# Optimization experiments

Measured on AMD Instinct MI355X. Metric: run time of the kernel, lower is better.

Reference implementation:

```python
import jax, jax.numpy as jnp
import numpy as np
import math

DEPTH = 6
D_MODEL = 512
N_HEADS = 8
D_HEAD = D_MODEL // N_HEADS
D_FF = 2048
SEQ_LEN = 2048
VOCAB = 256
B, T = 2, 2048
EPS = 1e-5


def setup_inputs() -> dict:
    key = jax.random.key(0)
    ks = jax.random.split(key, 16)
    std = 0.02
    std_proj = 0.02 / math.sqrt(2 * DEPTH)
    inp = {
        "x": jax.random.randint(ks[0], (B, T), 0, VOCAB, dtype=jnp.int64)
             if jax.config.jax_enable_x64 else
             jax.random.randint(ks[0], (B, T), 0, VOCAB, dtype=jnp.int32),
        "tok_emb": std * jax.random.normal(ks[1], (VOCAB, D_MODEL), jnp.float32),
        "pos_emb": std * jax.random.normal(ks[2], (SEQ_LEN, D_MODEL), jnp.float32),
        "qkv_w": std * jax.random.normal(ks[3], (DEPTH, 3 * D_MODEL, D_MODEL), jnp.float32),
        "proj_w": std_proj * jax.random.normal(ks[4], (DEPTH, D_MODEL, D_MODEL), jnp.float32),
        "ln1_w": jnp.ones((DEPTH, D_MODEL), jnp.float32),
        "ln1_b": jnp.zeros((DEPTH, D_MODEL), jnp.float32),
        "ln2_w": jnp.ones((DEPTH, D_MODEL), jnp.float32),
        "ln2_b": jnp.zeros((DEPTH, D_MODEL), jnp.float32),
        "fc1_w": std * jax.random.normal(ks[5], (DEPTH, D_FF, D_MODEL), jnp.float32),
        "fc2_w": std_proj * jax.random.normal(ks[6], (DEPTH, D_MODEL, D_FF), jnp.float32),
        "lnf_w": jnp.ones((D_MODEL,), jnp.float32),
        "lnf_b": jnp.zeros((D_MODEL,), jnp.float32),
        "head_w": std * jax.random.normal(ks[7], (VOCAB, D_MODEL), jnp.float32),
    }
    return inp


def _layernorm(x, w, b):
    mu = jnp.mean(x, axis=-1, keepdims=True)
    var = jnp.mean(jnp.square(x - mu), axis=-1, keepdims=True)
    return (x - mu) * jax.lax.rsqrt(var + EPS) * w + b


def _attention(x, qkv_w, proj_w):
    Bq, Tq, d = x.shape
    qkv = jnp.einsum('btd,ed->bte', x, qkv_w)  # [B,T,3d]
    q, k, v = jnp.split(qkv, 3, axis=-1)
    def split(t):
        return t.reshape(Bq, Tq, N_HEADS, D_HEAD).transpose(0, 2, 1, 3)  # [B,H,T,Dh]
    q, k, v = split(q), split(k), split(v)
    scores = jnp.einsum('bhqd,bhkd->bhqk', q, k) / math.sqrt(D_HEAD)
    mask = jnp.tril(jnp.ones((Tq, Tq), dtype=bool))
    scores = jnp.where(mask, scores, -jnp.inf)
    attn = jax.nn.softmax(scores, axis=-1)
    out = jnp.einsum('bhqk,bhkd->bhqd', attn, v)
    out = out.transpose(0, 2, 1, 3).reshape(Bq, Tq, d)
    return jnp.einsum('btd,ed->bte', out, proj_w)


def reference(x, tok_emb, pos_emb, qkv_w, proj_w, ln1_w, ln1_b, ln2_w, ln2_b,
              fc1_w, fc2_w, lnf_w, lnf_b, head_w):
    Tq = x.shape[1]
    h = tok_emb[x] + pos_emb[:Tq][None, :, :]  # [B,T,d]
    for l in range(DEPTH):
        a = _attention(_layernorm(h, ln1_w[l], ln1_b[l]), qkv_w[l], proj_w[l])
        h = h + a
        m = _layernorm(h, ln2_w[l], ln2_b[l])
        m = jax.nn.gelu(jnp.einsum('btd,fd->btf', m, fc1_w[l]), approximate=False)
        h = h + jnp.einsum('btf,df->btd', m, fc2_w[l])
    h = _layernorm(h, lnf_w, lnf_b)
    return jnp.einsum('btd,vd->btv', h, head_w)  # [B,T,VOCAB]
```

## Files before the change

### kernel.cpp

```cpp
#include <hip/hip_runtime.h>
#include <hip/hip_bf16.h>
#include <math.h>

typedef __hip_bfloat16 bf16;
typedef __attribute__((ext_vector_type(8))) short short8;
typedef __attribute__((ext_vector_type(4))) float f32x4;

#define DEPTH 6
#define DM    512
#define NH    8
#define DH    64
#define DFF   2048
#define TSEQ  2048
#define BATCH 2
#define ROWS  (BATCH*TSEQ)
#define NVOCAB 256

#define Q3_K_OFF  2097152
#define Q3_VT_OFF 4194304

constexpr size_t SZ_QKV  = (size_t)DEPTH * 3 * DM * DM;
constexpr size_t SZ_PROJ = (size_t)DEPTH * DM * DM;
constexpr size_t SZ_FC1  = (size_t)DEPTH * DFF * DM;
constexpr size_t SZ_FC2  = SZ_FC1;
constexpr size_t SZ_HEAD = (size_t)NVOCAB * DM;
constexpr size_t SZ_ALL  = SZ_QKV + SZ_PROJ + SZ_FC1 + SZ_FC2 + SZ_HEAD;

#define GLDS(gp, lp) __builtin_amdgcn_global_load_lds( \
    (const __attribute__((address_space(1))) void*)(gp), \
    (__attribute__((address_space(3))) void*)(lp), 16, 0, 0)

__device__ __forceinline__ short f2bs(float x) {
    union { bf16 b; short s; } u; u.b = __float2bfloat16(x); return u.s;
}

__global__ __launch_bounds__(256) void w2b_all(const float* __restrict__ q,
    const float* __restrict__ p, const float* __restrict__ f1,
    const float* __restrict__ f2, const float* __restrict__ hw, bf16* __restrict__ dst)
{
    size_t i = ((size_t)blockIdx.x * 256 + threadIdx.x) * 8;
    const float* s; size_t off;
    if      (i < SZ_QKV)                               { s = q;  off = 0; }
    else if (i < SZ_QKV + SZ_PROJ)                     { s = p;  off = SZ_QKV; }
    else if (i < SZ_QKV + SZ_PROJ + SZ_FC1)            { s = f1; off = SZ_QKV + SZ_PROJ; }
    else if (i < SZ_QKV + SZ_PROJ + SZ_FC1 + SZ_FC2)   { s = f2; off = SZ_QKV + SZ_PROJ + SZ_FC1; }
    else                                               { s = hw; off = SZ_QKV + SZ_PROJ + SZ_FC1 + SZ_FC2; }
    float4 f0 = *(const float4*)(s + (i - off));
    float4 f1v = *(const float4*)(s + (i - off) + 4);
    short8 o;
    o[0] = f2bs(f0.x); o[1] = f2bs(f0.y); o[2] = f2bs(f0.z); o[3] = f2bs(f0.w);
    o[4] = f2bs(f1v.x); o[5] = f2bs(f1v.y); o[6] = f2bs(f1v.z); o[7] = f2bs(f1v.w);
    *(short8*)((short*)dst + i) = o;
}

__global__ __launch_bounds__(256) void emb_kernel(const int* __restrict__ x,
    const float* __restrict__ tok, const float* __restrict__ pos, float* __restrict__ h)
{
    int i = blockIdx.x * 256 + threadIdx.x;
    int d = i & (DM - 1);
    int r = i >> 9;
    int t = r & (TSEQ - 1);
    h[i] = tok[x[r] * DM + d] + pos[t * DM + d];
}

__global__ __launch_bounds__(256) void ln_kernel(const float* __restrict__ x,
    const float* __restrict__ w, const float* __restrict__ b, bf16* __restrict__ out)
{
    int row = blockIdx.x * 4 + (threadIdx.x >> 6);
    int lane = threadIdx.x & 63;
    const float* xr = x + (size_t)row * DM;

    float4 v0 = *(const float4*)(xr + lane * 4);
    float4 v1 = *(const float4*)(xr + 256 + lane * 4);

    float s = v0.x + v0.y + v0.z + v0.w + v1.x + v1.y + v1.z + v1.w;
    #pragma unroll
    for (int m = 1; m < 64; m <<= 1) s += __shfl_xor(s, m, 64);
    float mu = s * (1.f / DM);

    float var = (v0.x-mu)*(v0.x-mu) + (v0.y-mu)*(v0.y-mu) + (v0.z-mu)*(v0.z-mu)
              + (v0.w-mu)*(v0.w-mu) + (v1.x-mu)*(v1.x-mu) + (v1.y-mu)*(v1.y-mu)
              + (v1.z-mu)*(v1.z-mu) + (v1.w-mu)*(v1.w-mu);
    #pragma unroll
    for (int m = 1; m < 64; m <<= 1) var += __shfl_xor(var, m, 64);
    float rstd = rsqrtf(var * (1.f / DM) + 1e-5f);

    float4 w0 = *(const float4*)(w + lane * 4);
    float4 w1 = *(const float4*)(w + 256 + lane * 4);
    float4 b0 = *(const float4*)(b + lane * 4);
    float4 b1 = *(const float4*)(b + 256 + lane * 4);

    short4 o0, o1;
    o0.x = f2bs((v0.x - mu) * rstd * w0.x + b0.x);
    o0.y = f2bs((v0.y - mu) * rstd * w0.y + b0.y);
    o0.z = f2bs((v0.z - mu) * rstd * w0.z + b0.z);
    o0.w = f2bs((v0.w - mu) * rstd * w0.w + b0.w);
    o1.x = f2bs((v1.x - mu) * rstd * w1.x + b1.x);
    o1.y = f2bs((v1.y - mu) * rstd * w1.y + b1.y);
    o1.z = f2bs((v1.z - mu) * rstd * w1.z + b1.z);
    o1.w = f2bs((v1.w - mu) * rstd * w1.w + b1.w);
    *(short4*)(out + (size_t)row * DM + lane * 4) = o0;
    *(short4*)(out + (size_t)row * DM + 256 + lane * 4) = o1;
}

template<int EPI, typename WT>
__global__ __launch_bounds__(256) void mfma_gemm(const bf16* __restrict__ A,
    const WT* __restrict__ W, void* __restrict__ Cv, int M, int N, int K)
{
    __shared__ short As[128 * 32];
    __shared__ short Bs[128 * 32];
    int tid = threadIdx.x;
    int bm0 = blockIdx.y * 128, bn0 = blockIdx.x * 128;
    int lane = tid & 63, w = tid >> 6;
    int wr = (w >> 1) * 64, wc = (w & 1) * 64;
    int fr = lane & 15, fk = (lane >> 4) * 8;

    f32x4 acc[4][4] = {};

    for (int k0 = 0; k0 < K; k0 += 32) {
        #pragma unroll
        for (int it = 0; it < 2; it++) {
            int c = it * 256 + tid;
            int row = c >> 2, kc = (c & 3) * 8;
            GLDS((const short*)A + (size_t)(bm0 + row) * K + k0 + kc, &As[c * 8]);
        }
        if constexpr (sizeof(WT) == 2) {
            #pragma unroll
            for (int it = 0; it < 2; it++) {
                int c = it * 256 + tid;
                int row = c >> 2, kc = (c & 3) * 8;
                GLDS((const short*)W + (size_t)(bn0 + row) * K + k0 + kc, &Bs[c * 8]);
            }
        } else {
            #pragma unroll
            for (int it = 0; it < 2; it++) {
                int c = it * 256 + tid;
                int row = c >> 2, kc = (c & 3) * 8;
                const float* wp = (const float*)W + (size_t)(bn0 + row) * K + k0 + kc;
                float4 f0 = *(const float4*)wp;
                float4 f1 = *(const float4*)(wp + 4);
                short8 p;
                p[0] = f2bs(f0.x); p[1] = f2bs(f0.y); p[2] = f2bs(f0.z); p[3] = f2bs(f0.w);
                p[4] = f2bs(f1.x); p[5] = f2bs(f1.y); p[6] = f2bs(f1.z); p[7] = f2bs(f1.w);
                *(short8*)&Bs[c * 8] = p;
            }
        }
        __syncthreads();

        short8 af[4], bfr[4];
        #pragma unroll
        for (int i = 0; i < 4; i++)
            af[i] = *(short8*)&As[(wr + i * 16 + fr) * 32 + fk];
        #pragma unroll
        for (int j = 0; j < 4; j++)
            bfr[j] = *(short8*)&Bs[(wc + j * 16 + fr) * 32 + fk];
        #pragma unroll
        for (int i = 0; i < 4; i++)
            #pragma unroll
            for (int j = 0; j < 4; j++)
                acc[i][j] = __builtin_amdgcn_mfma_f32_16x16x32_bf16(
                    af[i], bfr[j], acc[i][j], 0, 0, 0);
        __syncthreads();
    }

    int cr = (lane >> 4) * 4, cc = lane & 15;
    #pragma unroll
    for (int i = 0; i < 4; i++)
        #pragma unroll
        for (int j = 0; j < 4; j++)
            #pragma unroll
            for (int r = 0; r < 4; r++) {
                int m = bm0 + wr + i * 16 + cr + r;
                int n = bn0 + wc + j * 16 + cc;
                float v = acc[i][j][r];
                if (EPI == 4) {
                    short* q3s = (short*)Cv;
                    short sv = f2bs(v);
                    if (n < 512)
                        q3s[(size_t)m * 512 + n] = sv;
                    else if (n < 1024)
                        q3s[Q3_K_OFF + (size_t)m * 512 + (n - 512)] = sv;
                    else {
                        int bb = m >> 11, key = m & 2047;
                        int hd = (n - 1024) >> 6, dim = (n - 1024) & 63;
                        q3s[Q3_VT_OFF + (((size_t)(bb * 8 + hd) * 64 + dim) << 11) + key] = sv;
                    }
                } else {
                    size_t o = (size_t)m * N + n;
                    if (EPI == 0)      ((bf16*)Cv)[o] = __float2bfloat16(v);
                    else if (EPI == 1) ((float*)Cv)[o] += v;
                    else if (EPI == 2) ((bf16*)Cv)[o] =
                        __float2bfloat16(0.5f * v * (1.0f + erff(v * 0.70710678118654752f)));
                    else               ((float*)Cv)[o] = v;
                }
            }
}

template<int EPI, typename WT>
__global__ __launch_bounds__(256) void mfma_gemm_n64(const bf16* __restrict__ A,
    const WT* __restrict__ W, void* __restrict__ Cv, int M, int N, int K, int ldb)
{
    __shared__ short As[128 * 32];
    __shared__ short Bs[64 * 32];
    int tid = threadIdx.x;
    int bm0 = blockIdx.y * 128, bn0 = blockIdx.x * 64;
    int lane = tid & 63, w = tid >> 6;
    int wm = (w & 1) * 64, wn = (w >> 1) * 32;
    int fr = lane & 15, fk = (lane >> 4) * 8;

    f32x4 acc[4][2] = {};

    for (int k0 = 0; k0 < K; k0 += 32) {
        #pragma unroll
        for (int it = 0; it < 2; it++) {
            int c = it * 256 + tid;
            int row = c >> 2, kc = (c & 3) * 8;
            GLDS((const short*)A + (size_t)(bm0 + row) * K + k0 + kc, &As[c * 8]);
        }
        if constexpr (sizeof(WT) == 2) {
            int row = tid >> 2, kc = (tid & 3) * 8;
            GLDS((const short*)W + (size_t)(bn0 + row) * ldb + k0 + kc, &Bs[tid * 8]);
        } else {
            int row = tid >> 2, kc = (tid & 3) * 8;
            const float* wp = (const float*)W + (size_t)(bn0 + row) * ldb + k0 + kc;
            float4 f0 = *(const float4*)wp;
            float4 f1 = *(const float4*)(wp + 4);
            short8 p;
            p[0] = f2bs(f0.x); p[1] = f2bs(f0.y); p[2] = f2bs(f0.z); p[3] = f2bs(f0.w);
            p[4] = f2bs(f1.x); p[5] = f2bs(f1.y); p[6] = f2bs(f1.z); p[7] = f2bs(f1.w);
            *(short8*)&Bs[tid * 8] = p;
        }
        __syncthreads();

        short8 af[4], bfr[2];
        #pragma unroll
        for (int i = 0; i < 4; i++)
            af[i] = *(short8*)&As[(wm + i * 16 + fr) * 32 + fk];
        #pragma unroll
        for (int j = 0; j < 2; j++)
            bfr[j] = *(short8*)&Bs[(wn + j * 16 + fr) * 32 + fk];
        #pragma unroll
        for (int i = 0; i < 4; i++)
            #pragma unroll
            for (int j = 0; j < 2; j++)
                acc[i][j] = __builtin_amdgcn_mfma_f32_16x16x32_bf16(
                    af[i], bfr[j], acc[i][j], 0, 0, 0);
        __syncthreads();
    }

    int cr = (lane >> 4) * 4, cc = lane & 15;
    #pragma unroll
    for (int i = 0; i < 4; i++)
        #pragma unroll
        for (int j = 0; j < 2; j++)
            #pragma unroll
            for (int r = 0; r < 4; r++) {
                int m = bm0 + wm + i * 16 + cr + r;
                int n = bn0 + wn + j * 16 + cc;
                size_t o = (size_t)m * N + n;
                float v = acc[i][j][r];
                if (EPI == 0)      ((bf16*)Cv)[o] = __float2bfloat16(v);
                else if (EPI == 1) ((float*)Cv)[o] += v;
                else if (EPI == 2) ((bf16*)Cv)[o] =
                    __float2bfloat16(0.5f * v * (1.0f + erff(v * 0.70710678118654752f)));
                else               ((float*)Cv)[o] = v;
            }
}

__device__ __forceinline__ int pswz(int row, int col) {
    return row * 136 + ((((col >> 3) + row) & 15) << 3) + (col & 7);
}

__global__ __launch_bounds__(256) void fattn_kernel(const short* __restrict__ q3,
    bf16* __restrict__ out)
{
    __shared__ __align__(16) short Ks[128 * 72];
    __shared__ __align__(16) short Vt[64 * 136];
    __shared__ __align__(16) short Ps[4][16 * 136];

    int tid = threadIdx.x;
    int lane = tid & 63, w = tid >> 6;
    int quad = lane >> 4, cl = lane & 15;
    int bh = blockIdx.y;
    int b = bh >> 3, hd = bh & 7;
    int bx = blockIdx.x;
    int qt = b ? bx : (31 - bx);
    int q0 = qt * 64;
    const short* Qb = q3;
    const short* Kb = q3 + Q3_K_OFF + (size_t)b * 2048 * 512 + hd * 64;
    const short* Vb = q3 + Q3_VT_OFF + (size_t)bh * 64 * 2048;
    short* Pw = &Ps[w][0];

    short8 qf[2];
    {
        const short* qrow = Qb + (size_t)(b * 2048 + q0 + w * 16 + cl) * 512 + hd * 64;
        qf[0] = *(const short8*)(qrow + quad * 8);
        qf[1] = *(const short8*)(qrow + 32 + quad * 8);
    }

    float l_r[4] = {0.f, 0.f, 0.f, 0.f};
    f32x4 o_acc[4] = {};

    int nkt = (q0 + 64 + 127) >> 7;

    for (int kt = 0; kt < nkt; kt++) {
        int k0 = kt * 128;
        __syncthreads();
        #pragma unroll
        for (int it = 0; it < 2; it++) {
            int c = it * 512 + tid * 2;
            int row = c >> 3, cc = c & 7;
            const short* src = Kb + (size_t)(k0 + row) * 512 + cc * 8;
            *(short8*)&Ks[row * 72 + cc * 8] = *(const short8*)src;
            *(short8*)&Ks[row * 72 + cc * 8 + 8] = *(const short8*)(src + 8);
        }
        #pragma unroll
        for (int it = 0; it < 2; it++) {
            int c = it * 512 + tid * 2;
            int row = c >> 4, cc = c & 15;
            const short* src = Vb + (size_t)row * 2048 + k0 + cc * 8;
            *(short8*)&Vt[row * 136 + cc * 8] = *(const short8*)src;
            *(short8*)&Vt[row * 136 + cc * 8 + 8] = *(const short8*)(src + 8);
        }
        __syncthreads();

        f32x4 s[8];
        #pragma unroll
        for (int j = 0; j < 8; j++) {
            int key = j * 16 + cl;
            short8 kf0 = *(short8*)&Ks[key * 72 + quad * 8];
            short8 kf1 = *(short8*)&Ks[key * 72 + 32 + quad * 8];
            f32x4 a = {};
            a = __builtin_amdgcn_mfma_f32_16x16x32_bf16(qf[0], kf0, a, 0, 0, 0);
            a = __builtin_amdgcn_mfma_f32_16x16x32_bf16(qf[1], kf1, a, 0, 0, 0);
            s[j] = a;
        }

        int grow = q0 + w * 16 + quad * 4;
        bool last = (kt == nkt - 1);
        #pragma unroll
        for (int j = 0; j < 8; j++)
            #pragma unroll
            for (int r = 0; r < 4; r++) {
                bool masked = last && (k0 + j * 16 + cl) > (grow + r);
                float p = masked ? 0.f : __expf(s[j][r] * 0.125f);
                s[j][r] = p;
                l_r[r] += p;
            }

        #pragma unroll
        for (int j = 0; j < 8; j++) {
            int key = j * 16 + cl;
            #pragma unroll
            for (int r = 0; r < 4; r++)
                Pw[pswz(quad * 4 + r, key)] = f2bs(s[j][r]);
        }
        short8 pf[4];
        #pragma unroll
        for (int c = 0; c < 4; c++)
            pf[c] = *(short8*)&Pw[pswz(cl, c * 32 + quad * 8)];

        #pragma unroll
        for (int j = 0; j < 4; j++) {
            int dim = j * 16 + cl;
            #pragma unroll
            for (int c = 0; c < 4; c++) {
                short8 vf = *(short8*)&Vt[dim * 136 + c * 32 + quad * 8];
                o_acc[j] = __builtin_amdgcn_mfma_f32_16x16x32_bf16(
                    pf[c], vf, o_acc[j], 0, 0, 0);
            }
        }
    }

    int grow = q0 + w * 16 + quad * 4;
    #pragma unroll
    for (int r = 0; r < 4; r++) {
        float l = l_r[r];
        #pragma unroll
        for (int m = 1; m < 16; m <<= 1) l += __shfl_xor(l, m, 64);
        float inv = 1.f / l;
        #pragma unroll
        for (int j = 0; j < 4; j++)
            out[(size_t)(b * TSEQ + grow + r) * DM + hd * DH + j * 16 + cl] =
                __float2bfloat16(o_acc[j][r] * inv);
    }
}

template<typename WT>
static void run_model(const int* x, const float* tok, const float* pos,
    const WT* qkvw, const WT* projw,
    const float* ln1w, const float* ln1b, const float* ln2w, const float* ln2b,
    const WT* fc1w, const WT* fc2w, const float* lnfw, const float* lnfb,
    const WT* headw, float* h, bf16* xn, bf16* q3, float* dout, hipStream_t stream)
{
    emb_kernel<<<ROWS * DM / 256, 256, 0, stream>>>(x, tok, pos, h);

    for (int l = 0; l < DEPTH; l++) {
        ln_kernel<<<ROWS / 4, 256, 0, stream>>>(h, ln1w + l * DM, ln1b + l * DM, xn);
        mfma_gemm<4, WT><<<dim3(3 * DM / 128, ROWS / 128), 256, 0, stream>>>(
            xn, qkvw + (size_t)l * 3 * DM * DM, q3, ROWS, 3 * DM, DM);
        fattn_kernel<<<dim3(TSEQ / 64, BATCH * NH), 256, 0, stream>>>((short*)q3, xn);
        mfma_gemm_n64<1, WT><<<dim3(DM / 64, ROWS / 128), 256, 0, stream>>>(
            xn, projw + (size_t)l * DM * DM, h, ROWS, DM, DM, DM);
        ln_kernel<<<ROWS / 4, 256, 0, stream>>>(h, ln2w + l * DM, ln2b + l * DM, xn);
        for (int p = 0; p < 2; p++) {
            mfma_gemm<2, WT><<<dim3(1024 / 128, ROWS / 128), 256, 0, stream>>>(
                xn, fc1w + (size_t)l * DFF * DM + (size_t)p * 1024 * DM,
                q3, ROWS, 1024, DM);
            mfma_gemm_n64<1, WT><<<dim3(DM / 64, ROWS / 128), 256, 0, stream>>>(
                q3, fc2w + (size_t)l * DM * DFF + (size_t)p * 1024,
                h, ROWS, DM, 1024, DFF);
        }
    }

    ln_kernel<<<ROWS / 4, 256, 0, stream>>>(h, lnfw, lnfb, xn);
    mfma_gemm_n64<3, WT><<<dim3(NVOCAB / 64, ROWS / 128), 256, 0, stream>>>(
        xn, headw, dout, ROWS, NVOCAB, DM, DM);
}

extern "C" void kernel_launch(void* const* d_in, const int* in_sizes, int n_in,
                              void* d_out, int out_size, void* d_ws, size_t ws_size,
                              hipStream_t stream)
{
    const int*   x     = (const int*)d_in[0];
    const float* tok   = (const float*)d_in[1];
    const float* pos   = (const float*)d_in[2];
    const float* qkvw  = (const float*)d_in[3];
    const float* projw = (const float*)d_in[4];
    const float* ln1w  = (const float*)d_in[5];
    const float* ln1b  = (const float*)d_in[6];
    const float* ln2w  = (const float*)d_in[7];
    const float* ln2b  = (const float*)d_in[8];
    const float* fc1w  = (const float*)d_in[9];
    const float* fc2w  = (const float*)d_in[10];
    const float* lnfw  = (const float*)d_in[11];
    const float* lnfb  = (const float*)d_in[12];
    const float* headw = (const float*)d_in[13];

    char* ws = (char*)d_ws;
    float* h  = (float*)ws;
    bf16*  xn = (bf16*)(ws + (8u << 20));
    bf16*  q3 = (bf16*)(ws + (12u << 20));

    const size_t need = ((size_t)24 << 20) + 2 * SZ_ALL;

    if (ws_size >= need) {
        bf16* wb = (bf16*)(ws + (24u << 20));
        w2b_all<<<SZ_ALL / 2048, 256, 0, stream>>>(qkvw, projw, fc1w, fc2w, headw, wb);
        const bf16* qkvwb  = wb;
        const bf16* projwb = qkvwb + SZ_QKV;
        const bf16* fc1wb  = projwb + SZ_PROJ;
        const bf16* fc2wb  = fc1wb + SZ_FC1;
        const bf16* headwb = fc2wb + SZ_FC2;
        run_model<bf16>(x, tok, pos, qkvwb, projwb, ln1w, ln1b, ln2w, ln2b,
                        fc1wb, fc2wb, lnfw, lnfb, headwb,
                        h, xn, q3, (float*)d_out, stream);
    } else {
        run_model<float>(x, tok, pos, qkvw, projw, ln1w, ln1b, ln2w, ln2b,
                         fc1w, fc2w, lnfw, lnfb, headw,
                         h, xn, q3, (float*)d_out, stream);
    }
}
```

Baseline: 1.298 ms.

## Run full-width MLP GEMMs via a dedicated hidden buffer; coalesce attention tile loads

When the workspace is large enough, the MLP now stores the whole 4096x2048 bf16 hidden activation and runs one fc1 GEMM and one fc2 GEMM with K=2048, instead of two half-width chunks that each do a read-modify-write of the residual. This halves the fc GEMM launches and the residual traffic. The attention kernel's K/V tile loads are rewritten so each thread issues single 16-byte loads with adjacent threads on adjacent addresses, rather than paired loads with a stride. The cost is 16 MB of extra workspace, and the old path is kept as a fallback.

```diff
diff --git a/kernel.cpp b/kernel.cpp
--- a/kernel.cpp
+++ b/kernel.cpp
@@ -302,25 +302,23 @@
     f32x4 o_acc[4] = {};
 
     int nkt = (q0 + 64 + 127) >> 7;
+    int krow0 = tid >> 3, kcc = tid & 7;
+    int vrow0 = tid >> 4, vcc = tid & 15;
 
     for (int kt = 0; kt < nkt; kt++) {
         int k0 = kt * 128;
         __syncthreads();
         #pragma unroll
-        for (int it = 0; it < 2; it++) {
-            int c = it * 512 + tid * 2;
-            int row = c >> 3, cc = c & 7;
-            const short* src = Kb + (size_t)(k0 + row) * 512 + cc * 8;
-            *(short8*)&Ks[row * 72 + cc * 8] = *(const short8*)src;
-            *(short8*)&Ks[row * 72 + cc * 8 + 8] = *(const short8*)(src + 8);
-        }
-        #pragma unroll
-        for (int it = 0; it < 2; it++) {
-            int c = it * 512 + tid * 2;
-            int row = c >> 4, cc = c & 15;
-            const short* src = Vb + (size_t)row * 2048 + k0 + cc * 8;
-            *(short8*)&Vt[row * 136 + cc * 8] = *(const short8*)src;
-            *(short8*)&Vt[row * 136 + cc * 8 + 8] = *(const short8*)(src + 8);
+        for (int it = 0; it < 4; it++) {
+            int row = it * 32 + krow0;
+            *(short8*)&Ks[row * 72 + kcc * 8] =
+                *(const short8*)(Kb + (size_t)(k0 + row) * 512 + kcc * 8);
+        }
+        #pragma unroll
+        for (int it = 0; it < 4; it++) {
+            int row = it * 16 + vrow0;
+            *(short8*)&Vt[row * 136 + vcc * 8] =
+                *(const short8*)(Vb + (size_t)row * 2048 + k0 + vcc * 8);
         }
         __syncthreads();
 
@@ -391,7 +389,8 @@
     const WT* qkvw, const WT* projw,
     const float* ln1w, const float* ln1b, const float* ln2w, const float* ln2b,
     const WT* fc1w, const WT* fc2w, const float* lnfw, const float* lnfb,
-    const WT* headw, float* h, bf16* xn, bf16* q3, float* dout, hipStream_t stream)
+    const WT* headw, float* h, bf16* xn, bf16* q3, bf16* hid16,
+    float* dout, hipStream_t stream)
 {
     emb_kernel<<<ROWS * DM / 256, 256, 0, stream>>>(x, tok, pos, h);
 
@@ -403,13 +402,20 @@
         mfma_gemm_n64<1, WT><<<dim3(DM / 64, ROWS / 128), 256, 0, stream>>>(
             xn, projw + (size_t)l * DM * DM, h, ROWS, DM, DM, DM);
         ln_kernel<<<ROWS / 4, 256, 0, stream>>>(h, ln2w + l * DM, ln2b + l * DM, xn);
-        for (int p = 0; p < 2; p++) {
-            mfma_gemm<2, WT><<<dim3(1024 / 128, ROWS / 128), 256, 0, stream>>>(
-                xn, fc1w + (size_t)l * DFF * DM + (size_t)p * 1024 * DM,
-                q3, ROWS, 1024, DM);
+        if (hid16) {
+            mfma_gemm<2, WT><<<dim3(DFF / 128, ROWS / 128), 256, 0, stream>>>(
+                xn, fc1w + (size_t)l * DFF * DM, hid16, ROWS, DFF, DM);
             mfma_gemm_n64<1, WT><<<dim3(DM / 64, ROWS / 128), 256, 0, stream>>>(
-                q3, fc2w + (size_t)l * DM * DFF + (size_t)p * 1024,
-                h, ROWS, DM, 1024, DFF);
+                hid16, fc2w + (size_t)l * DM * DFF, h, ROWS, DM, DFF, DFF);
+        } else {
+            for (int p = 0; p < 2; p++) {
+                mfma_gemm<2, WT><<<dim3(1024 / 128, ROWS / 128), 256, 0, stream>>>(
+                    xn, fc1w + (size_t)l * DFF * DM + (size_t)p * 1024 * DM,
+                    q3, ROWS, 1024, DM);
+                mfma_gemm_n64<1, WT><<<dim3(DM / 64, ROWS / 128), 256, 0, stream>>>(
+                    q3, fc2w + (size_t)l * DM * DFF + (size_t)p * 1024,
+                    h, ROWS, DM, 1024, DFF);
+            }
         }
     }
 
@@ -442,10 +448,14 @@
     bf16*  xn = (bf16*)(ws + (8u << 20));
     bf16*  q3 = (bf16*)(ws + (12u << 20));
 
-    const size_t need = ((size_t)24 << 20) + 2 * SZ_ALL;
-
-    if (ws_size >= need) {
-        bf16* wb = (bf16*)(ws + (24u << 20));
+    const size_t wb_off = (size_t)24 << 20;
+    const size_t hid_off = wb_off + 2 * SZ_ALL;
+    const size_t need1 = hid_off;
+    const size_t need2 = hid_off + ((size_t)16 << 20);
+
+    if (ws_size >= need1) {
+        bf16* wb = (bf16*)(ws + wb_off);
+        bf16* hid16 = (ws_size >= need2) ? (bf16*)(ws + hid_off) : (bf16*)nullptr;
         w2b_all<<<SZ_ALL / 2048, 256, 0, stream>>>(qkvw, projw, fc1w, fc2w, headw, wb);
         const bf16* qkvwb  = wb;
         const bf16* projwb = qkvwb + SZ_QKV;
@@ -454,10 +464,10 @@
         const bf16* headwb = fc2wb + SZ_FC2;
         run_model<bf16>(x, tok, pos, qkvwb, projwb, ln1w, ln1b, ln2w, ln2b,
                         fc1wb, fc2wb, lnfw, lnfb, headwb,
-                        h, xn, q3, (float*)d_out, stream);
+                        h, xn, q3, hid16, (float*)d_out, stream);
     } else {
         run_model<float>(x, tok, pos, qkvw, projw, ln1w, ln1b, ln2w, ln2b,
                          fc1w, fc2w, lnfw, lnfb, headw,
-                         h, xn, q3, (float*)d_out, stream);
-    }
-}
+                         h, xn, q3, (bf16*)nullptr, (float*)d_out, stream);
+    }
+}
```

Result: faster. 1.190 ms (-8.3%).
